# Kernel tuning notes

Measured on AMD Instinct MI355X. Metric: run time of the kernel, lower is better.

## Reference

```python
import jax, jax.numpy as jnp
import numpy as np

FP8_MAX = 448.0
SCALE_EPS = 1e-6


def setup_inputs() -> dict:
    key = jax.random.key(0)
    k1, k2, k3 = jax.random.split(key, 3)
    B, S, D_IN, D_OUT = 4, 2048, 4096, 4096
    x = jax.random.normal(k1, (B, S, D_IN), dtype=jnp.float32)
    weight = jax.random.normal(k2, (D_OUT, D_IN), dtype=jnp.float32) * 0.02
    bias = jax.random.normal(k3, (D_OUT,), dtype=jnp.float32) * 0.01
    return {"x": x, "weight": weight, "bias": bias}


def _quantize_weight(weight):
    # per-output-row amax -> scale (computed in fp32, stored via fp16 round-trip as in _quantize_weight)
    w = weight.astype(jnp.float32)
    max_abs = jnp.max(jnp.abs(w), axis=1, keepdims=True)          # [out, 1]
    scale = jnp.maximum(max_abs / FP8_MAX, SCALE_EPS)
    scale = scale.astype(jnp.float16).astype(jnp.float32)          # fp16 storage of scale, copied back to fp32 buffer
    w_fp8 = jnp.clip(w / scale, -FP8_MAX, FP8_MAX).astype(jnp.float8_e4m3fn)
    return w_fp8, scale


def reference(x, weight, bias):
    out_features, in_features = weight.shape
    w_fp8, w_scale = _quantize_weight(weight)                      # [out,in] fp8, [out,1] f32

    x2d = x.reshape(-1, in_features)                               # [T, in]
    act_abs = jnp.max(jnp.abs(x2d), axis=1, keepdims=True)         # per-row amax [T,1]
    act_scale = jnp.maximum(act_abs / FP8_MAX, SCALE_EPS).astype(jnp.float32)
    x_fp8 = jnp.clip(x2d / act_scale.astype(x.dtype), -FP8_MAX, FP8_MAX).astype(jnp.float8_e4m3fn)

    # torch._scaled_mm: (x_fp8 @ w_fp8^T) * act_scale * weight_scale^T + bias(bf16), out in bf16
    acc = jnp.matmul(x_fp8.astype(jnp.float32), w_fp8.astype(jnp.float32).T)  # [T, out]
    out = acc * act_scale * w_scale.T
    out = out + bias.astype(jnp.bfloat16).astype(jnp.float32)
    out = out.astype(jnp.bfloat16).astype(x.dtype)
    return out.reshape(*x.shape[:-1], out_features)
```

## Files before the change

kernel.cpp:

```cpp
#include <hip/hip_runtime.h>
#include <hip/hip_fp16.h>
#include <stdint.h>

#define FP8_MAX_V 448.0f
#define BM 128
#define BN 128
#define BKB 128

typedef float floatx4 __attribute__((ext_vector_type(4)));
typedef int intx4 __attribute__((ext_vector_type(4)));
typedef int intx8 __attribute__((ext_vector_type(8)));

#define WAITVM(n)                                              \
  do {                                                         \
    asm volatile("s_waitcnt vmcnt(" #n ")" ::: "memory");      \
    __builtin_amdgcn_sched_barrier(0);                         \
  } while (0)
#define BARRIER()                                              \
  do {                                                         \
    __builtin_amdgcn_sched_barrier(0);                         \
    __builtin_amdgcn_s_barrier();                              \
    __builtin_amdgcn_sched_barrier(0);                         \
  } while (0)

__device__ __forceinline__ float bf16_rne(float v) {
  uint32_t u = __float_as_uint(v);
  u = (u + 0x7fffu + ((u >> 16) & 1u)) & 0xffff0000u;
  return __uint_as_float(u);
}

__device__ __forceinline__ uint32_t pack4_fp8(float a, float b, float c, float d) {
  int p = 0;
  p = __builtin_amdgcn_cvt_pk_fp8_f32(a, b, p, false);
  p = __builtin_amdgcn_cvt_pk_fp8_f32(c, d, p, true);
  return (uint32_t)p;
}

__device__ __forceinline__ void gload_lds16(const uint8_t* g, uint8_t* l) {
  __builtin_amdgcn_global_load_lds(
      (const __attribute__((address_space(1))) uint32_t*)g,
      (__attribute__((address_space(3))) uint32_t*)l,
      16, 0, 0);
}

template <bool FP16RT>
__global__ __launch_bounds__(256) void quant_rows_kernel(
    const float* __restrict__ in, uint8_t* __restrict__ out8,
    float* __restrict__ scales, int K) {
  const int row = blockIdx.x;
  const int tid = threadIdx.x;
  const float* rp = in + (size_t)row * K;

  float4 v[4];
  float amax = 0.f;
#pragma unroll
  for (int i = 0; i < 4; ++i) {
    v[i] = ((const float4*)rp)[i * 256 + tid];
    amax = fmaxf(amax, fmaxf(fmaxf(fabsf(v[i].x), fabsf(v[i].y)),
                             fmaxf(fabsf(v[i].z), fabsf(v[i].w))));
  }
#pragma unroll
  for (int off = 32; off; off >>= 1) amax = fmaxf(amax, __shfl_xor(amax, off));
  __shared__ float red[4];
  if ((tid & 63) == 0) red[tid >> 6] = amax;
  __syncthreads();
  amax = fmaxf(fmaxf(red[0], red[1]), fmaxf(red[2], red[3]));

  float scale = fmaxf(amax / FP8_MAX_V, 1e-6f);
  if (FP16RT) scale = __half2float(__float2half(scale));
  if (tid == 0) scales[row] = scale;

  uint32_t* op = (uint32_t*)(out8 + (size_t)row * K);
#pragma unroll
  for (int i = 0; i < 4; ++i) {
    float qa = fminf(fmaxf(v[i].x / scale, -FP8_MAX_V), FP8_MAX_V);
    float qb = fminf(fmaxf(v[i].y / scale, -FP8_MAX_V), FP8_MAX_V);
    float qc = fminf(fmaxf(v[i].z / scale, -FP8_MAX_V), FP8_MAX_V);
    float qd = fminf(fmaxf(v[i].w / scale, -FP8_MAX_V), FP8_MAX_V);
    op[i * 256 + tid] = pack4_fp8(qa, qb, qc, qd);
  }
}

__global__ __launch_bounds__(256) void gemm_fp8_kernel(
    const uint8_t* __restrict__ A8, const uint8_t* __restrict__ B8,
    const float* __restrict__ asc, const float* __restrict__ wsc,
    const float* __restrict__ bias, float* __restrict__ out,
    int M, int N, int K) {
  __shared__ __align__(16) uint8_t As[2][BM * BKB];
  __shared__ __align__(16) uint8_t Bs[2][BN * BKB];

  const int tid = threadIdx.x;
  const int lane = tid & 63;
  const int wid = tid >> 6;
  const int wr = wid >> 1;
  const int wc = wid & 1;

  const int ntn = N / BN;
  const int bm = blockIdx.x / ntn;
  const int bn = blockIdx.x % ntn;

  floatx4 acc[4][4] = {};

  const int srow = tid >> 3;
  const int sc_log = (tid & 7) ^ (srow & 7);
  const uint8_t* ga0 = A8 + (size_t)(bm * BM + srow) * K + sc_log * 16;
  const uint8_t* gb0 = B8 + (size_t)(bn * BN + srow) * K + sc_log * 16;
  const size_t rstep = (size_t)32 * K;

  const int fr = lane & 15;
  const int hi = lane >> 4;
  const int fsw = fr & 7;
  const int cls = ((2 * hi) ^ fsw) * 16;
  const int chs = ((2 * hi + 1) ^ fsw) * 16;

  auto stage = [&](int buf, int k0) {
    uint8_t* lA = As[buf] + tid * 16;
    uint8_t* lB = Bs[buf] + tid * 16;
#pragma unroll
    for (int i = 0; i < 4; ++i) gload_lds16(ga0 + i * rstep + k0, lA + i * 4096);
#pragma unroll
    for (int i = 0; i < 4; ++i) gload_lds16(gb0 + i * rstep + k0, lB + i * 4096);
  };

  auto compute = [&](int buf) {
    const uint8_t* Ab = As[buf];
    const uint8_t* Bb = Bs[buf];
    intx8 a[4], b[4];
#pragma unroll
    for (int m = 0; m < 4; ++m) {
      const uint8_t* p = Ab + (size_t)(wr * 64 + m * 16 + fr) * BKB;
      intx4 lo = *(const intx4*)(p + cls);
      intx4 hh = *(const intx4*)(p + chs);
      a[m] = (intx8){lo.x, lo.y, lo.z, lo.w, hh.x, hh.y, hh.z, hh.w};
    }
#pragma unroll
    for (int n = 0; n < 4; ++n) {
      const uint8_t* p = Bb + (size_t)(wc * 64 + n * 16 + fr) * BKB;
      intx4 lo = *(const intx4*)(p + cls);
      intx4 hh = *(const intx4*)(p + chs);
      b[n] = (intx8){lo.x, lo.y, lo.z, lo.w, hh.x, hh.y, hh.z, hh.w};
    }
#pragma unroll
    for (int m = 0; m < 4; ++m)
#pragma unroll
      for (int n = 0; n < 4; ++n)
        acc[m][n] = __builtin_amdgcn_mfma_scale_f32_16x16x128_f8f6f4(
            a[m], b[n], acc[m][n], 0, 0, 0, 0x7F7F7F7F, 0, 0x7F7F7F7F);
  };

  const int NT = K / BKB;
  stage(0, 0);
  stage(1, BKB);

  for (int t = 0; t < NT; ++t) {
    const int cur = t & 1;
    if (t + 1 < NT) WAITVM(8); else WAITVM(0);
    BARRIER();
    compute(cur);
    BARRIER();
    if (t + 2 < NT) stage(cur, (t + 2) * BKB);
  }

  const int rbase = bm * BM + wr * 64;
  const int cbase = bn * BN + wc * 64;
#pragma unroll
  for (int n = 0; n < 4; ++n) {
    const int col = cbase + n * 16 + fr;
    const float wv = wsc[col];
    const float bb = bf16_rne(bias[col]);
#pragma unroll
    for (int m = 0; m < 4; ++m) {
      const int r0 = rbase + m * 16 + hi * 4;
#pragma unroll
      for (int r = 0; r < 4; ++r) {
        const int row = r0 + r;
        float v = (acc[m][n][r] * asc[row]) * wv + bb;
        out[(size_t)row * N + col] = bf16_rne(v);
      }
    }
  }
}

extern "C" void kernel_launch(void* const* d_in, const int* in_sizes, int n_in,
                              void* d_out, int out_size, void* d_ws, size_t ws_size,
                              hipStream_t stream) {
  const float* x = (const float*)d_in[0];
  const float* w = (const float*)d_in[1];
  const float* bias = (const float*)d_in[2];
  float* out = (float*)d_out;

  const int N = in_sizes[2];
  const int K = in_sizes[1] / N;
  const int M = in_sizes[0] / K;

  uint8_t* x8 = (uint8_t*)d_ws;
  uint8_t* w8 = x8 + (size_t)M * K;
  float* asc = (float*)(w8 + (size_t)N * K);
  float* wsc = asc + M;
  (void)ws_size; (void)n_in; (void)out_size;

  quant_rows_kernel<false><<<M, 256, 0, stream>>>(x, x8, asc, K);
  quant_rows_kernel<true><<<N, 256, 0, stream>>>(w, w8, wsc, K);
  gemm_fp8_kernel<<<(M / BM) * (N / BN), 256, 0, stream>>>(x8, w8, asc, wsc, bias, out, M, N, K);
}
```

Before: 196.4 us.

## Load B fragments directly into registers and halve LDS for occupancy

The weight (B) tile no longer goes through shared memory. Each wave loads its own B MFMA fragments straight from global memory into registers, double-buffered one K-tile ahead, and the loop is unrolled by two. Only the A tile stays staged in LDS, which halves LDS use, and launch_bounds now requests 2 blocks per CU to raise occupancy. In exchange, B data is fetched twice per block (once by each of the two waves sharing a column group). B load latency is hidden only one tile ahead, and register pressure grows from the second B fragment set.

```diff
diff --git a/kernel.cpp b/kernel.cpp
--- a/kernel.cpp
+++ b/kernel.cpp
@@ -81,13 +81,12 @@
   }
 }
 
-__global__ __launch_bounds__(256) void gemm_fp8_kernel(
+__global__ __launch_bounds__(256, 2) void gemm_fp8_kernel(
     const uint8_t* __restrict__ A8, const uint8_t* __restrict__ B8,
     const float* __restrict__ asc, const float* __restrict__ wsc,
     const float* __restrict__ bias, float* __restrict__ out,
     int M, int N, int K) {
   __shared__ __align__(16) uint8_t As[2][BM * BKB];
-  __shared__ __align__(16) uint8_t Bs[2][BN * BKB];
 
   const int tid = threadIdx.x;
   const int lane = tid & 63;
@@ -104,7 +103,6 @@
   const int srow = tid >> 3;
   const int sc_log = (tid & 7) ^ (srow & 7);
   const uint8_t* ga0 = A8 + (size_t)(bm * BM + srow) * K + sc_log * 16;
-  const uint8_t* gb0 = B8 + (size_t)(bn * BN + srow) * K + sc_log * 16;
   const size_t rstep = (size_t)32 * K;
 
   const int fr = lane & 15;
@@ -113,19 +111,27 @@
   const int cls = ((2 * hi) ^ fsw) * 16;
   const int chs = ((2 * hi + 1) ^ fsw) * 16;
 
-  auto stage = [&](int buf, int k0) {
+  const uint8_t* gBb = B8 + (size_t)(bn * BN + wc * 64 + fr) * K + hi * 32;
+
+  auto stageA = [&](int buf, int k0) {
     uint8_t* lA = As[buf] + tid * 16;
-    uint8_t* lB = Bs[buf] + tid * 16;
 #pragma unroll
     for (int i = 0; i < 4; ++i) gload_lds16(ga0 + i * rstep + k0, lA + i * 4096);
-#pragma unroll
-    for (int i = 0; i < 4; ++i) gload_lds16(gb0 + i * rstep + k0, lB + i * 4096);
   };
 
-  auto compute = [&](int buf) {
+  auto loadB = [&](intx8* bb, int k0) {
+#pragma unroll
+    for (int n = 0; n < 4; ++n) {
+      const uint8_t* p = gBb + (size_t)(n * 16) * K + k0;
+      intx4 lo = *(const intx4*)p;
+      intx4 hh = *(const intx4*)(p + 16);
+      bb[n] = (intx8){lo.x, lo.y, lo.z, lo.w, hh.x, hh.y, hh.z, hh.w};
+    }
+  };
+
+  auto computeA = [&](int buf, const intx8* bb) {
     const uint8_t* Ab = As[buf];
-    const uint8_t* Bb = Bs[buf];
-    intx8 a[4], b[4];
+    intx8 a[4];
 #pragma unroll
     for (int m = 0; m < 4; ++m) {
       const uint8_t* p = Ab + (size_t)(wr * 64 + m * 16 + fr) * BKB;
@@ -134,31 +140,33 @@
       a[m] = (intx8){lo.x, lo.y, lo.z, lo.w, hh.x, hh.y, hh.z, hh.w};
     }
 #pragma unroll
-    for (int n = 0; n < 4; ++n) {
-      const uint8_t* p = Bb + (size_t)(wc * 64 + n * 16 + fr) * BKB;
-      intx4 lo = *(const intx4*)(p + cls);
-      intx4 hh = *(const intx4*)(p + chs);
-      b[n] = (intx8){lo.x, lo.y, lo.z, lo.w, hh.x, hh.y, hh.z, hh.w};
-    }
-#pragma unroll
     for (int m = 0; m < 4; ++m)
 #pragma unroll
       for (int n = 0; n < 4; ++n)
         acc[m][n] = __builtin_amdgcn_mfma_scale_f32_16x16x128_f8f6f4(
-            a[m], b[n], acc[m][n], 0, 0, 0, 0x7F7F7F7F, 0, 0x7F7F7F7F);
+            a[m], bb[n], acc[m][n], 0, 0, 0, 0x7F7F7F7F, 0, 0x7F7F7F7F);
   };
 
   const int NT = K / BKB;
-  stage(0, 0);
-  stage(1, BKB);
-
-  for (int t = 0; t < NT; ++t) {
-    const int cur = t & 1;
-    if (t + 1 < NT) WAITVM(8); else WAITVM(0);
-    BARRIER();
-    compute(cur);
-    BARRIER();
-    if (t + 2 < NT) stage(cur, (t + 2) * BKB);
+  intx8 b0[4], b1[4];
+  stageA(0, 0);
+  loadB(b0, 0);
+  stageA(1, BKB);
+
+  for (int t = 0; t < NT; t += 2) {
+    if (t + 1 < NT) WAITVM(4); else WAITVM(0);
+    BARRIER();
+    if (t + 1 < NT) loadB(b1, (t + 1) * BKB);
+    computeA(0, b0);
+    BARRIER();
+    if (t + 2 < NT) stageA(0, (t + 2) * BKB);
+
+    if (t + 2 < NT) WAITVM(4); else WAITVM(0);
+    BARRIER();
+    if (t + 2 < NT) loadB(b0, (t + 2) * BKB);
+    computeA(1, b1);
+    BARRIER();
+    if (t + 3 < NT) stageA(1, (t + 3) * BKB);
   }
 
   const int rbase = bm * BM + wr * 64;
```

Result: slower. 339.4 us (+72.9%).

## Single-buffer GEMM B tile for occupancy and merge quantization launches

Applied to the files above, without the earlier changes.

The B operand tile in LDS goes from double to single buffering, cutting shared memory per block so more blocks can be resident on a CU, with a launch-bounds hint of two. B for the next step is now loaded right after the compute barrier and waited on at the top of the next iteration, while A keeps its two-stage prefetch. The activation and weight quantization kernels are fused into one launch that picks its source by block index. The trade-off is that B global-load latency is less hidden within a block and now depends on other resident blocks to cover it.

```diff
diff --git a/kernel.cpp b/kernel.cpp
--- a/kernel.cpp
+++ b/kernel.cpp
@@ -43,13 +43,17 @@
       16, 0, 0);
 }
 
-template <bool FP16RT>
-__global__ __launch_bounds__(256) void quant_rows_kernel(
-    const float* __restrict__ in, uint8_t* __restrict__ out8,
-    float* __restrict__ scales, int K) {
-  const int row = blockIdx.x;
+__global__ __launch_bounds__(256) void quant_all_kernel(
+    const float* __restrict__ x, const float* __restrict__ w,
+    uint8_t* __restrict__ x8, uint8_t* __restrict__ w8,
+    float* __restrict__ asc, float* __restrict__ wsc, int M, int K) {
+  const int blk = blockIdx.x;
+  const bool isW = blk >= M;
+  const int row = isW ? (blk - M) : blk;
+  const float* rp = (isW ? w : x) + (size_t)row * K;
+  uint8_t* out8 = (isW ? w8 : x8) + (size_t)row * K;
+  float* scp = (isW ? wsc : asc) + row;
   const int tid = threadIdx.x;
-  const float* rp = in + (size_t)row * K;
 
   float4 v[4];
   float amax = 0.f;
@@ -67,10 +71,10 @@
   amax = fmaxf(fmaxf(red[0], red[1]), fmaxf(red[2], red[3]));
 
   float scale = fmaxf(amax / FP8_MAX_V, 1e-6f);
-  if (FP16RT) scale = __half2float(__float2half(scale));
-  if (tid == 0) scales[row] = scale;
-
-  uint32_t* op = (uint32_t*)(out8 + (size_t)row * K);
+  if (isW) scale = __half2float(__float2half(scale));
+  if (tid == 0) *scp = scale;
+
+  uint32_t* op = (uint32_t*)out8;
 #pragma unroll
   for (int i = 0; i < 4; ++i) {
     float qa = fminf(fmaxf(v[i].x / scale, -FP8_MAX_V), FP8_MAX_V);
@@ -81,13 +85,13 @@
   }
 }
 
-__global__ __launch_bounds__(256) void gemm_fp8_kernel(
+__global__ __launch_bounds__(256, 2) void gemm_fp8_kernel(
     const uint8_t* __restrict__ A8, const uint8_t* __restrict__ B8,
     const float* __restrict__ asc, const float* __restrict__ wsc,
     const float* __restrict__ bias, float* __restrict__ out,
     int M, int N, int K) {
   __shared__ __align__(16) uint8_t As[2][BM * BKB];
-  __shared__ __align__(16) uint8_t Bs[2][BN * BKB];
+  __shared__ __align__(16) uint8_t Bs[BN * BKB];
 
   const int tid = threadIdx.x;
   const int lane = tid & 63;
@@ -113,18 +117,19 @@
   const int cls = ((2 * hi) ^ fsw) * 16;
   const int chs = ((2 * hi + 1) ^ fsw) * 16;
 
-  auto stage = [&](int buf, int k0) {
+  auto stageA = [&](int buf, int k0) {
     uint8_t* lA = As[buf] + tid * 16;
-    uint8_t* lB = Bs[buf] + tid * 16;
 #pragma unroll
     for (int i = 0; i < 4; ++i) gload_lds16(ga0 + i * rstep + k0, lA + i * 4096);
+  };
+  auto stageB = [&](int k0) {
+    uint8_t* lB = Bs + tid * 16;
 #pragma unroll
     for (int i = 0; i < 4; ++i) gload_lds16(gb0 + i * rstep + k0, lB + i * 4096);
   };
 
   auto compute = [&](int buf) {
     const uint8_t* Ab = As[buf];
-    const uint8_t* Bb = Bs[buf];
     intx8 a[4], b[4];
 #pragma unroll
     for (int m = 0; m < 4; ++m) {
@@ -135,7 +140,7 @@
     }
 #pragma unroll
     for (int n = 0; n < 4; ++n) {
-      const uint8_t* p = Bb + (size_t)(wc * 64 + n * 16 + fr) * BKB;
+      const uint8_t* p = Bs + (size_t)(wc * 64 + n * 16 + fr) * BKB;
       intx4 lo = *(const intx4*)(p + cls);
       intx4 hh = *(const intx4*)(p + chs);
       b[n] = (intx8){lo.x, lo.y, lo.z, lo.w, hh.x, hh.y, hh.z, hh.w};
@@ -149,16 +154,17 @@
   };
 
   const int NT = K / BKB;
-  stage(0, 0);
-  stage(1, BKB);
+  stageA(0, 0);
+  stageB(0);
+  stageA(1, BKB);
 
   for (int t = 0; t < NT; ++t) {
-    const int cur = t & 1;
-    if (t + 1 < NT) WAITVM(8); else WAITVM(0);
+    if (t + 1 < NT) WAITVM(4); else WAITVM(0);
     BARRIER();
-    compute(cur);
+    compute(t & 1);
     BARRIER();
-    if (t + 2 < NT) stage(cur, (t + 2) * BKB);
+    if (t + 1 < NT) stageB((t + 1) * BKB);
+    if (t + 2 < NT) stageA(t & 1, (t + 2) * BKB);
   }
 
   const int rbase = bm * BM + wr * 64;
@@ -199,7 +205,6 @@
   float* wsc = asc + M;
   (void)ws_size; (void)n_in; (void)out_size;
 
-  quant_rows_kernel<false><<<M, 256, 0, stream>>>(x, x8, asc, K);
-  quant_rows_kernel<true><<<N, 256, 0, stream>>>(w, w8, wsc, K);
+  quant_all_kernel<<<M + N, 256, 0, stream>>>(x, w, x8, w8, asc, wsc, M, K);
   gemm_fp8_kernel<<<(M / BM) * (N / BN), 256, 0, stream>>>(x8, w8, asc, wsc, bias, out, M, N, K);
 }
```

New measurement: 193.5 us. No clear change (-1.5%).
